# Kernel tuning notes

Measured on AMD Instinct MI355X. Metric: run time of the kernel, lower is better.

The kernel has to match this reference:

```python
import jax, jax.numpy as jnp
import numpy as np

D = 1024       # d_model
DR = 1024      # d_rec
FFN = 4096     # ffn_inner
K = 4          # conv_kernel
B, T = 2, 4096
CHUNK = 64
EPS = 1e-6


def setup_inputs() -> dict:
    key = jax.random.key(0)
    ks = jax.random.split(key, 8)
    s = lambda k, shape, scale: jax.random.normal(k, shape, jnp.float32) * scale
    db = np.zeros((DR,), np.float32)
    q = DR // 4
    db[:q] = -2.2
    db[q:3 * q] = 0.0
    db[3 * q:] = 4.6
    return {
        "x": s(ks[0], (B, T, D), 1.0),
        "pre_norm_w": jnp.ones((D,), jnp.float32),
        "conv_w": s(ks[1], (D, 1, K), 0.3),
        "conv_b": jnp.zeros((D,), jnp.float32),
        "w_a": s(ks[2], (DR, D), 0.02),
        "w_i": s(ks[3], (DR, D), 0.02),
        "w_v": s(ks[4], (DR, D), 0.02),
        "out_proj_w": s(ks[5], (D, DR), 0.02),
        "decay_bias": jnp.asarray(db),
        "ffn_norm_w": jnp.ones((D,), jnp.float32),
        "w_gate_up": s(ks[6], (2 * FFN, D), 0.02),
        "w_down": s(ks[7], (D, FFN), 0.02),
    }


def rmsnorm(x, w):
    return x * jax.lax.rsqrt(jnp.mean(x * x, axis=-1, keepdims=True) + EPS) * w


def lin(x, w):  # nn.Linear weight layout (out, in)
    return jnp.einsum('btd,od->bto', x, w)


def causal_conv(h, w, b):
    # depthwise causal conv: h (B,T,D), w (D,1,K)
    hc = jnp.transpose(h, (0, 2, 1))  # (B,D,T)
    out = jax.lax.conv_general_dilated(
        hc, w, window_strides=(1,), padding=[(K - 1, 0)],
        dimension_numbers=('NCH', 'OIH', 'NCH'), feature_group_count=D)
    return jnp.transpose(out, (0, 2, 1)) + b


def chunked_scan(a, v):
    b, s, d = a.shape
    pad = (-s) % CHUNK
    af = jnp.pad(a, ((0, 0), (0, pad), (0, 0)), constant_values=1.0)
    vf = jnp.pad(v, ((0, 0), (0, pad), (0, 0)))
    n = (s + pad) // CHUNK
    dc = af.reshape(b, n, CHUNK, d)
    vc = vf.reshape(b, n, CHUNK, d)
    cum_decay = jnp.exp(jnp.cumsum(jnp.log(jnp.clip(dc, 1e-10)), axis=2))
    intra = cum_decay * jnp.cumsum(vc / jnp.clip(cum_decay, 1e-10), axis=2)

    def step(state, xs):
        cd, it = xs  # (B,CHUNK,d) each
        cs = it + cd * state[:, None, :]
        return cs[:, -1], cs

    _, states = jax.lax.scan(
        step, jnp.zeros((b, d), jnp.float32),
        (jnp.transpose(cum_decay, (1, 0, 2, 3)), jnp.transpose(intra, (1, 0, 2, 3))))
    return jnp.transpose(states, (1, 0, 2, 3)).reshape(b, n * CHUNK, d)[:, :s]


def reference(x, pre_norm_w, conv_w, conv_b, w_a, w_i, w_v, out_proj_w,
              decay_bias, ffn_norm_w, w_gate_up, w_down):
    h = rmsnorm(x, pre_norm_w)
    h = causal_conv(h, conv_w, conv_b)
    a = jax.nn.sigmoid(lin(h, w_a) + decay_bias)
    i_gate = jax.nn.sigmoid(lin(h, w_i))
    v = lin(h, w_v)
    input_signal = jnp.sqrt(jnp.clip(1.0 - a * a, 1e-8)) * (i_gate * v)
    rec_out = chunked_scan(a, input_signal).astype(x.dtype)
    x = x + lin(rec_out, out_proj_w)
    hn = rmsnorm(x, ffn_norm_w)
    gu = lin(hn, w_gate_up)
    gate, up = gu[..., :FFN], gu[..., FFN:]
    x = x + lin(jax.nn.silu(gate) * up, w_down)
    return x
```

## Files before the change

### kernel.cpp

```cpp
#include <hip/hip_runtime.h>

typedef __bf16 bf16_t;
typedef bf16_t bf16x4 __attribute__((ext_vector_type(4)));
typedef bf16_t bf16x8 __attribute__((ext_vector_type(8)));
typedef float f32x4 __attribute__((ext_vector_type(4)));

#define DD 1024
#define TT 4096

__device__ __forceinline__ void gload16(const void* g, void* l) {
    __builtin_amdgcn_global_load_lds(
        (const __attribute__((address_space(1))) void*)g,
        (__attribute__((address_space(3))) void*)l, 16, 0, 0);
}

__global__ __launch_bounds__(256) void cvt3_k(const float* __restrict__ s0,
                                              const float* __restrict__ s1,
                                              const float* __restrict__ s2,
                                              bf16_t* __restrict__ d0,
                                              bf16_t* __restrict__ d1,
                                              bf16_t* __restrict__ d2) {
    const int i = (blockIdx.x * 256 + threadIdx.x) * 4;
    const float* s; bf16_t* d; int off;
    if (i < 1048576)            { s = s0; d = d0; off = i; }
    else if (i < 2097152)       { s = s1; d = d1; off = i - 1048576; }
    else                        { s = s2; d = d2; off = i - 2097152; }
    const float4 v = *(const float4*)(s + off);
    bf16x4 o;
    o[0] = (bf16_t)v.x; o[1] = (bf16_t)v.y; o[2] = (bf16_t)v.z; o[3] = (bf16_t)v.w;
    *(bf16x4*)(d + off) = o;
}

__global__ __launch_bounds__(256) void cvt_ilv2_k(const float* __restrict__ wi,
                                                  const float* __restrict__ wv,
                                                  bf16_t* __restrict__ wivb,
                                                  const float* __restrict__ wgu,
                                                  bf16_t* __restrict__ wgub) {
    const int i = (blockIdx.x * 256 + threadIdx.x) * 4;
    const float* src; bf16_t* dst; int idx;
    if (i < 2097152) {
        idx = i;
        const int rp = idx >> 10, k = idx & 1023, c = rp >> 1;
        src = ((rp & 1) ? wv : wi) + (long)c * 1024 + k;
        dst = wivb + idx;
    } else {
        idx = i - 2097152;
        const int rp = idx >> 10, k = idx & 1023, c = rp >> 1;
        src = ((rp & 1) ? (wgu + 4194304) : wgu) + (long)c * 1024 + k;
        dst = wgub + idx;
    }
    const float4 v = *(const float4*)src;
    bf16x4 o;
    o[0] = (bf16_t)v.x; o[1] = (bf16_t)v.y; o[2] = (bf16_t)v.z; o[3] = (bf16_t)v.w;
    *(bf16x4*)dst = o;
}

__global__ __launch_bounds__(256) void rmsnorm_k(const float* __restrict__ x,
                                                 const float* __restrict__ w,
                                                 bf16_t* __restrict__ ob) {
    const long row = blockIdx.x;
    const float* xr = x + row * DD;
    const int t4 = threadIdx.x * 4;
    float4 v = *(const float4*)(xr + t4);
    float s = v.x*v.x + v.y*v.y + v.z*v.z + v.w*v.w;
    #pragma unroll
    for (int off = 1; off < 64; off <<= 1) s += __shfl_xor(s, off);
    __shared__ float red[4];
    if ((threadIdx.x & 63) == 0) red[threadIdx.x >> 6] = s;
    __syncthreads();
    float tot = red[0] + red[1] + red[2] + red[3];
    float sc = rsqrtf(tot * (1.0f / DD) + 1e-6f);
    float4 wv = *(const float4*)(w + t4);
    bf16x4 o;
    o[0] = (bf16_t)(v.x*sc*wv.x); o[1] = (bf16_t)(v.y*sc*wv.y);
    o[2] = (bf16_t)(v.z*sc*wv.z); o[3] = (bf16_t)(v.w*sc*wv.w);
    *(bf16x4*)(ob + row * DD + t4) = o;
}

__global__ __launch_bounds__(256) void conv_k(const bf16_t* __restrict__ h,
                                              const float* __restrict__ cw,
                                              const float* __restrict__ cb,
                                              bf16_t* __restrict__ hc) {
    const long idx = (long)blockIdx.x * 256 + threadIdx.x;
    const int d = (int)(idx & (DD - 1));
    const long bt = idx >> 10;
    const int t = (int)(bt & (TT - 1));
    const float w0 = cw[d*4+0], w1 = cw[d*4+1], w2 = cw[d*4+2], w3 = cw[d*4+3];
    const bf16_t* hp = h + bt * DD + d;
    float acc = cb[d] + (float)hp[0] * w3;
    if (t >= 1) acc += (float)hp[-DD]     * w2;
    if (t >= 2) acc += (float)hp[-2*DD]   * w1;
    if (t >= 3) acc += (float)hp[-3*DD]   * w0;
    hc[idx] = (bf16_t)acc;
}

__global__ __launch_bounds__(256) void scan1_k(const bf16_t* __restrict__ ap,
                                               const bf16_t* __restrict__ sp,
                                               float* __restrict__ cd63,
                                               float* __restrict__ i63) {
    const int d = blockIdx.x * 256 + threadIdx.x;
    const int c = blockIdx.y;
    const int b = blockIdx.z;
    const long rowbase = (long)b * TT + (long)c * 64;
    float cd = 1.0f, rs = 0.0f;
    for (int t = 0; t < 64; t++) {
        const long off = (rowbase + t) * DD + d;
        const float a = (float)ap[off];
        const float s = (float)sp[off];
        const float sig = __builtin_amdgcn_sqrtf(fmaxf(1.0f - a * a, 1e-8f)) * s;
        cd *= fmaxf(a, 1e-10f);
        rs = fmaf(sig, __builtin_amdgcn_rcpf(fmaxf(cd, 1e-10f)), rs);
    }
    const long o = ((long)b * 64 + c) * DD + d;
    cd63[o] = cd;
    i63[o]  = cd * rs;
}

__global__ __launch_bounds__(256) void scan2_k(const float* __restrict__ cd63,
                                               const float* __restrict__ i63,
                                               float* __restrict__ carry_in) {
    const int g = blockIdx.x * 256 + threadIdx.x;
    const int b = g >> 10, d = g & (DD - 1);
    float st = 0.0f;
    for (int c = 0; c < 64; c++) {
        const long o = ((long)b * 64 + c) * DD + d;
        carry_in[o] = st;
        st = i63[o] + cd63[o] * st;
    }
}

__global__ __launch_bounds__(256) void scan3_k(const bf16_t* __restrict__ ap,
                                               const bf16_t* __restrict__ sp,
                                               const float* __restrict__ carry_in,
                                               bf16_t* __restrict__ rec) {
    const int d = blockIdx.x * 256 + threadIdx.x;
    const int c = blockIdx.y;
    const int b = blockIdx.z;
    const long rowbase = (long)b * TT + (long)c * 64;
    const float carry = carry_in[((long)b * 64 + c) * DD + d];
    float cd = 1.0f, rs = 0.0f;
    for (int t = 0; t < 64; t++) {
        const long off = (rowbase + t) * DD + d;
        const float a = (float)ap[off];
        const float s = (float)sp[off];
        const float sig = __builtin_amdgcn_sqrtf(fmaxf(1.0f - a * a, 1e-8f)) * s;
        cd *= fmaxf(a, 1e-10f);
        rs = fmaf(sig, __builtin_amdgcn_rcpf(fmaxf(cd, 1e-10f)), rs);
        rec[off] = (bf16_t)(cd * (rs + carry));
    }
}

enum { EPI_SIGB = 0, EPI_ADDRES = 1, EPI_IV = 2, EPI_GU = 3 };

template<int EPI, int NREP>
__global__ __launch_bounds__(512, 2) void gemm2p_k(const bf16_t* __restrict__ Ag,
                                                   const bf16_t* __restrict__ Bg,
                                                   int M, int N, int K,
                                                   float* outF, bf16_t* outB,
                                                   const float* aux, int ldc) {
    constexpr int BN  = NREP * 64;
    constexpr int ASZ = 16384;
    constexpr int BSZ = BN * 64;
    constexpr int BUF = ASZ + BSZ;
    extern __shared__ bf16_t smem[];
    const int tid = threadIdx.x;
    const int l = tid & 63;
    const int w = tid >> 6;
    const int wm = w >> 2, wn = w & 3;

    const int gx = gridDim.x;
    const int gy = gridDim.y;
    const int lin = blockIdx.y * gx + blockIdx.x;
    long row0, col0;
    if ((gy & 7) == 0) {
        const int rpc = gy >> 3;
        const int q = lin >> 3;
        row0 = (long)((lin & 7) * rpc + q % rpc) * 256;
        col0 = (long)(q / rpc) * (long)BN;
    } else {
        row0 = (long)blockIdx.y * 256;
        col0 = (long)blockIdx.x * BN;
    }

    const int srow = l >> 3;
    const int scol = ((l & 7) ^ srow) * 8;
    const long aBase = row0 + srow;
    const long bBase = col0 + srow;
    const int R0a = w * 32;
    const int R0b = w * (BN / 8);

    const int NT = K >> 6;
    f32x4 acc[8][NREP] = {};

    const int lq2 = (l >> 4) * 16;
    const int rA = wm * 128 + (l & 15);
    const int rB = wn * (NREP * 16) + (l & 15);
    const int eA0 = rA * 64 + ((lq2 ^ ((rA & 7) << 4)) >> 1);
    const int eB0 = ASZ + rB * 64 + ((lq2 ^ ((rB & 7) << 4)) >> 1);

    #define STAGE_A(tt, off)                                                          \
        { const long kgk = (long)(tt) * 64 + scol;                                    \
          _Pragma("unroll")                                                           \
          for (int i = 0; i < 4; i++)                                                 \
              gload16(Ag + (aBase + R0a + i * 8) * (long)K + kgk,                     \
                      &smem[(off) + (R0a + i * 8) * 64]); }
    #define STAGE_B(tt, off)                                                          \
        { const long kgk = (long)(tt) * 64 + scol;                                    \
          _Pragma("unroll")                                                           \
          for (int i = 0; i < NREP; i++)                                              \
              gload16(Bg + (bBase + R0b + i * 8) * (long)K + kgk,                     \
                      &smem[(off) + ASZ + (R0b + i * 8) * 64]); }

    STAGE_A(0, 0); STAGE_B(0, 0);
    STAGE_A(1, BUF); STAGE_B(1, BUF);
    if constexpr (NREP == 4) { asm volatile("s_waitcnt vmcnt(8)" ::: "memory"); }
    else                     { asm volatile("s_waitcnt vmcnt(6)" ::: "memory"); }
    asm volatile("s_barrier" ::: "memory");

    bf16x8 pA[2][4], pB[2][NREP];
    #pragma unroll
    for (int kk = 0; kk < 2; kk++) {
        const int xo = kk * 32;
        #pragma unroll
        for (int n = 0; n < NREP; n++)
            pB[kk][n] = *(const bf16x8*)&smem[(eB0 ^ xo) + n * 1024];
        #pragma unroll
        for (int m = 0; m < 4; m++)
            pA[kk][m] = *(const bf16x8*)&smem[(eA0 ^ xo) + m * 1024];
    }

    for (int t = 0; t < NT; t++) {
        const int co = (t & 1) ? BUF : 0;
        const int oo = BUF - co;
        bf16x8 a1[2][4];

        __builtin_amdgcn_s_setprio(1);
        #pragma unroll
        for (int kk = 0; kk < 2; kk++)
            #pragma unroll
            for (int m = 0; m < 4; m++)
                #pragma unroll
                for (int n = 0; n < NREP; n++)
                    acc[m][n] = __builtin_amdgcn_mfma_f32_16x16x32_bf16(pA[kk][m], pB[kk][n], acc[m][n], 0, 0, 0);
        __builtin_amdgcn_s_setprio(0);
        #pragma unroll
        for (int kk = 0; kk < 2; kk++) {
            const int xo = kk * 32;
            #pragma unroll
            for (int m = 0; m < 4; m++)
                a1[kk][m] = *(const bf16x8*)&smem[co + (eA0 ^ xo) + 4096 + m * 1024];
        }
        asm volatile("s_barrier" ::: "memory");

        if (t + 2 < NT) { STAGE_A(t + 2, co); STAGE_B(t + 2, co); }
        __builtin_amdgcn_s_setprio(1);
        #pragma unroll
        for (int kk = 0; kk < 2; kk++)
            #pragma unroll
            for (int m = 0; m < 4; m++)
                #pragma unroll
                for (int n = 0; n < NREP; n++)
                    acc[m + 4][n] = __builtin_amdgcn_mfma_f32_16x16x32_bf16(a1[kk][m], pB[kk][n], acc[m + 4][n], 0, 0, 0);
        __builtin_amdgcn_s_setprio(0);
        if (t + 2 < NT) {
            if constexpr (NREP == 4) { asm volatile("s_waitcnt vmcnt(8)" ::: "memory"); }
            else                     { asm volatile("s_waitcnt vmcnt(6)" ::: "memory"); }
        } else if (t + 1 < NT) {
            asm volatile("s_waitcnt vmcnt(0)" ::: "memory");
        }
        asm volatile("s_barrier" ::: "memory");
        if (t + 1 < NT) {
            #pragma unroll
            for (int kk = 0; kk < 2; kk++) {
                const int xo = kk * 32;
                #pragma unroll
                for (int n = 0; n < NREP; n++)
                    pB[kk][n] = *(const bf16x8*)&smem[oo + (eB0 ^ xo) + n * 1024];
                #pragma unroll
                for (int m = 0; m < 4; m++)
                    pA[kk][m] = *(const bf16x8*)&smem[oo + (eA0 ^ xo) + m * 1024];
            }
        }
    }
    #undef STAGE_A
    #undef STAGE_B

    #pragma unroll
    for (int m = 0; m < 8; m++) {
        const long r0 = row0 + wm * 128 + m * 16 + (l >> 4) * 4;
        #pragma unroll
        for (int n = 0; n < NREP; n++) {
            const long cc = col0 + wn * (NREP * 16) + n * 16 + (l & 15);
            f32x4 v = acc[m][n];
            #pragma unroll
            for (int j = 0; j < 4; j++) {
                const long r = r0 + j;
                const float xv = v[j];
                if (EPI == EPI_SIGB) {
                    outB[r * ldc + cc] = (bf16_t)(1.0f / (1.0f + __expf(-(xv + aux[cc]))));
                } else if (EPI == EPI_ADDRES) {
                    outF[r * ldc + cc] = xv + aux[r * ldc + cc];
                } else if (EPI == EPI_IV) {
                    const float px = __shfl_xor(xv, 1);
                    if ((l & 1) == 0)
                        outB[r * ldc + (cc >> 1)] = (bf16_t)(px / (1.0f + __expf(-xv)));
                } else {
                    const float px = __shfl_xor(xv, 1);
                    if ((l & 1) == 0)
                        outB[r * ldc + (cc >> 1)] = (bf16_t)(xv / (1.0f + __expf(-xv)) * px);
                }
            }
        }
    }
}

extern "C" void kernel_launch(void* const* d_in, const int* in_sizes, int n_in,
                              void* d_out, int out_size, void* d_ws, size_t ws_size,
                              hipStream_t stream) {
    const float* x   = (const float*)d_in[0];
    const float* pnw = (const float*)d_in[1];
    const float* cw  = (const float*)d_in[2];
    const float* cb  = (const float*)d_in[3];
    const float* wa  = (const float*)d_in[4];
    const float* wi  = (const float*)d_in[5];
    const float* wv  = (const float*)d_in[6];
    const float* wop = (const float*)d_in[7];
    const float* db  = (const float*)d_in[8];
    const float* fnw = (const float*)d_in[9];
    const float* wgu = (const float*)d_in[10];
    const float* wdn = (const float*)d_in[11];
    float* out = (float*)d_out;

    char* ws = (char*)d_ws;
    bf16_t* wab   = (bf16_t*)(ws + 0);
    bf16_t* wivb  = (bf16_t*)(ws + 2097152);
    bf16_t* wopb  = (bf16_t*)(ws + 6291456);
    bf16_t* wgub  = (bf16_t*)(ws + 8388608);
    bf16_t* wdnb  = (bf16_t*)(ws + 25165824);
    bf16_t* hb    = (bf16_t*)(ws + 33554432);
    bf16_t* hn    = hb;
    bf16_t* hc    = (bf16_t*)(ws + 50331648);
    bf16_t* rec   = hc;
    bf16_t* a_b   = (bf16_t*)(ws + 67108864);
    bf16_t* s_b   = (bf16_t*)(ws + 100663296);
    bf16_t* act   = (bf16_t*)(ws + 67108864);
    float*  cd63  = (float*)(ws + 134217728);
    float*  i63   = (float*)(ws + 134742016);
    float*  carry = (float*)(ws + 135266304);

    const int LDS4 = 131072;
    const int LDS2 = 98304;
    hipFuncSetAttribute((const void*)gemm2p_k<EPI_SIGB, 2>,   hipFuncAttributeMaxDynamicSharedMemorySize, LDS2);
    hipFuncSetAttribute((const void*)gemm2p_k<EPI_IV, 4>,     hipFuncAttributeMaxDynamicSharedMemorySize, LDS4);
    hipFuncSetAttribute((const void*)gemm2p_k<EPI_ADDRES, 2>, hipFuncAttributeMaxDynamicSharedMemorySize, LDS2);
    hipFuncSetAttribute((const void*)gemm2p_k<EPI_GU, 4>,     hipFuncAttributeMaxDynamicSharedMemorySize, LDS4);

    cvt3_k    <<<6144, 256, 0, stream>>>(wa, wop, wdn, wab, wopb, wdnb);
    cvt_ilv2_k<<<10240, 256, 0, stream>>>(wi, wv, wivb, wgu, wgub);

    rmsnorm_k<<<8192, 256, 0, stream>>>(x, pnw, hb);
    conv_k<<<32768, 256, 0, stream>>>(hb, cw, cb, hc);

    gemm2p_k<EPI_SIGB, 2><<<dim3(8, 32), 512, LDS2, stream>>>(hc, wab,  8192, 1024, 1024,
                                                              nullptr, a_b, db, 1024);
    gemm2p_k<EPI_IV, 4>  <<<dim3(8, 32), 512, LDS4, stream>>>(hc, wivb, 8192, 2048, 1024,
                                                              nullptr, s_b, nullptr, 1024);
    scan1_k<<<dim3(4, 64, 2), 256, 0, stream>>>(a_b, s_b, cd63, i63);
    scan2_k<<<8, 256, 0, stream>>>(cd63, i63, carry);
    scan3_k<<<dim3(4, 64, 2), 256, 0, stream>>>(a_b, s_b, carry, rec);

    gemm2p_k<EPI_ADDRES, 2><<<dim3(8, 32), 512, LDS2, stream>>>(rec, wopb, 8192, 1024, 1024,
                                                                out, nullptr, x, 1024);
    rmsnorm_k<<<8192, 256, 0, stream>>>(out, fnw, hn);
    gemm2p_k<EPI_GU, 4><<<dim3(32, 32), 512, LDS4, stream>>>(hn, wgub, 8192, 8192, 1024,
                                                             nullptr, act, nullptr, 4096);
    gemm2p_k<EPI_ADDRES, 2><<<dim3(8, 32), 512, LDS2, stream>>>(act, wdnb, 8192, 1024, 4096,
                                                                out, nullptr, out, 1024);
}
```

Baseline: 436.8 us.

## Add 128x128-tile GEMM kernel for N=1024 projections to raise CU occupancy

Adds a new 256-thread GEMM kernel with 128x128 tiles, 64 KB LDS and two blocks per CU. It stages A and B separately with double buffering and uses an XCD-aware tile swizzle. The three GEMMs with N=1024 (decay gate, out-projection, down-projection) move to it, launching 512 blocks instead of 256. This is meant to fix poor CU fill from too few large tiles on 256 CUs, at the cost of less data reuse per tile and more total memory traffic.

```diff
diff --git a/kernel.cpp b/kernel.cpp
--- a/kernel.cpp
+++ b/kernel.cpp
@@ -314,6 +314,139 @@
     }
 }
 
+template<int EPI>
+__global__ __launch_bounds__(256, 2) void gemm2b_k(const bf16_t* __restrict__ Ag,
+                                                   const bf16_t* __restrict__ Bg,
+                                                   int M, int N, int K,
+                                                   float* outF, bf16_t* outB,
+                                                   const float* aux, int ldc) {
+    constexpr int ASZ = 8192;
+    constexpr int BUF = 16384;
+    extern __shared__ bf16_t smem[];
+    const int tid = threadIdx.x;
+    const int l = tid & 63;
+    const int w = tid >> 6;
+    const int wm = w >> 1, wn = w & 1;
+
+    const int gx = gridDim.x;
+    const int gy = gridDim.y;
+    const int lin = blockIdx.y * gx + blockIdx.x;
+    long row0, col0;
+    if ((gy & 7) == 0) {
+        const int rpc = gy >> 3;
+        const int q = lin >> 3;
+        row0 = (long)((lin & 7) * rpc + q % rpc) * 128;
+        col0 = (long)(q / rpc) * 128;
+    } else {
+        row0 = (long)blockIdx.y * 128;
+        col0 = (long)blockIdx.x * 128;
+    }
+
+    const int srow = l >> 3;
+    const int scol = ((l & 7) ^ srow) * 8;
+    const long aBase = row0 + srow;
+    const long bBase = col0 + srow;
+    const int R0 = w * 32;
+
+    const int NT = K >> 6;
+    f32x4 acc[4][4] = {};
+
+    const int lq2 = (l >> 4) * 16;
+    const int rA = wm * 64 + (l & 15);
+    const int rB = wn * 64 + (l & 15);
+    const int eA0 = rA * 64 + ((lq2 ^ ((rA & 7) << 4)) >> 1);
+    const int eB0 = ASZ + rB * 64 + ((lq2 ^ ((rB & 7) << 4)) >> 1);
+
+    #define ST_A(tt, off, i)                                                        \
+        gload16(Ag + (aBase + R0 + (i) * 8) * (long)K + (long)(tt) * 64 + scol,     \
+                &smem[(off) + (R0 + (i) * 8) * 64])
+    #define ST_B(tt, off, i)                                                        \
+        gload16(Bg + (bBase + R0 + (i) * 8) * (long)K + (long)(tt) * 64 + scol,     \
+                &smem[(off) + ASZ + (R0 + (i) * 8) * 64])
+    #define BAR asm volatile("s_barrier" ::: "memory")
+
+    #pragma unroll
+    for (int i = 0; i < 4; i++) ST_B(0, 0, i);
+    #pragma unroll
+    for (int i = 0; i < 4; i++) ST_A(0, 0, i);
+    #pragma unroll
+    for (int i = 0; i < 4; i++) ST_B(1, BUF, i);
+    asm volatile("s_waitcnt vmcnt(4)" ::: "memory");
+    BAR;
+
+    for (int t = 0; t < NT; t++) {
+        const int cur = (t & 1) * BUF;
+        const int oth = BUF - cur;
+        bf16x8 bk[4], af[4];
+
+        #pragma unroll
+        for (int n = 0; n < 4; n++)
+            bk[n] = *(const bf16x8*)&smem[cur + eB0 + n * 1024];
+        #pragma unroll
+        for (int m = 0; m < 4; m++)
+            af[m] = *(const bf16x8*)&smem[cur + eA0 + m * 1024];
+        if (t + 1 < NT) {
+            #pragma unroll
+            for (int i = 0; i < 4; i++) ST_A(t + 1, oth, i);
+        }
+        BAR;
+        __builtin_amdgcn_s_setprio(1);
+        #pragma unroll
+        for (int m = 0; m < 4; m++)
+            #pragma unroll
+            for (int n = 0; n < 4; n++)
+                acc[m][n] = __builtin_amdgcn_mfma_f32_16x16x32_bf16(af[m], bk[n], acc[m][n], 0, 0, 0);
+        __builtin_amdgcn_s_setprio(0);
+        BAR;
+
+        #pragma unroll
+        for (int n = 0; n < 4; n++)
+            bk[n] = *(const bf16x8*)&smem[cur + (eB0 ^ 32) + n * 1024];
+        #pragma unroll
+        for (int m = 0; m < 4; m++)
+            af[m] = *(const bf16x8*)&smem[cur + (eA0 ^ 32) + m * 1024];
+        BAR;
+        __builtin_amdgcn_s_setprio(1);
+        #pragma unroll
+        for (int m = 0; m < 4; m++)
+            #pragma unroll
+            for (int n = 0; n < 4; n++)
+                acc[m][n] = __builtin_amdgcn_mfma_f32_16x16x32_bf16(af[m], bk[n], acc[m][n], 0, 0, 0);
+        __builtin_amdgcn_s_setprio(0);
+        if (t + 2 < NT) {
+            #pragma unroll
+            for (int i = 0; i < 4; i++) ST_B(t + 2, cur, i);
+            asm volatile("s_waitcnt vmcnt(4)" ::: "memory");
+        } else {
+            asm volatile("s_waitcnt vmcnt(0)" ::: "memory");
+        }
+        BAR;
+    }
+    #undef ST_A
+    #undef ST_B
+    #undef BAR
+
+    #pragma unroll
+    for (int m = 0; m < 4; m++) {
+        const long r0 = row0 + wm * 64 + m * 16 + (l >> 4) * 4;
+        #pragma unroll
+        for (int n = 0; n < 4; n++) {
+            const long cc = col0 + wn * 64 + n * 16 + (l & 15);
+            f32x4 v = acc[m][n];
+            #pragma unroll
+            for (int j = 0; j < 4; j++) {
+                const long r = r0 + j;
+                const float xv = v[j];
+                if (EPI == EPI_SIGB) {
+                    outB[r * ldc + cc] = (bf16_t)(1.0f / (1.0f + __expf(-(xv + aux[cc]))));
+                } else {
+                    outF[r * ldc + cc] = xv + aux[r * ldc + cc];
+                }
+            }
+        }
+    }
+}
+
 extern "C" void kernel_launch(void* const* d_in, const int* in_sizes, int n_in,
                               void* d_out, int out_size, void* d_ws, size_t ws_size,
                               hipStream_t stream) {
@@ -349,11 +482,11 @@
     float*  carry = (float*)(ws + 135266304);
 
     const int LDS4 = 131072;
-    const int LDS2 = 98304;
-    hipFuncSetAttribute((const void*)gemm2p_k<EPI_SIGB, 2>,   hipFuncAttributeMaxDynamicSharedMemorySize, LDS2);
-    hipFuncSetAttribute((const void*)gemm2p_k<EPI_IV, 4>,     hipFuncAttributeMaxDynamicSharedMemorySize, LDS4);
-    hipFuncSetAttribute((const void*)gemm2p_k<EPI_ADDRES, 2>, hipFuncAttributeMaxDynamicSharedMemorySize, LDS2);
-    hipFuncSetAttribute((const void*)gemm2p_k<EPI_GU, 4>,     hipFuncAttributeMaxDynamicSharedMemorySize, LDS4);
+    const int LDSB = 65536;
+    hipFuncSetAttribute((const void*)gemm2p_k<EPI_IV, 4>,   hipFuncAttributeMaxDynamicSharedMemorySize, LDS4);
+    hipFuncSetAttribute((const void*)gemm2p_k<EPI_GU, 4>,   hipFuncAttributeMaxDynamicSharedMemorySize, LDS4);
+    hipFuncSetAttribute((const void*)gemm2b_k<EPI_SIGB>,    hipFuncAttributeMaxDynamicSharedMemorySize, LDSB);
+    hipFuncSetAttribute((const void*)gemm2b_k<EPI_ADDRES>,  hipFuncAttributeMaxDynamicSharedMemorySize, LDSB);
 
     cvt3_k    <<<6144, 256, 0, stream>>>(wa, wop, wdn, wab, wopb, wdnb);
     cvt_ilv2_k<<<10240, 256, 0, stream>>>(wi, wv, wivb, wgu, wgub);
@@ -361,19 +494,19 @@
     rmsnorm_k<<<8192, 256, 0, stream>>>(x, pnw, hb);
     conv_k<<<32768, 256, 0, stream>>>(hb, cw, cb, hc);
 
-    gemm2p_k<EPI_SIGB, 2><<<dim3(8, 32), 512, LDS2, stream>>>(hc, wab,  8192, 1024, 1024,
-                                                              nullptr, a_b, db, 1024);
-    gemm2p_k<EPI_IV, 4>  <<<dim3(8, 32), 512, LDS4, stream>>>(hc, wivb, 8192, 2048, 1024,
-                                                              nullptr, s_b, nullptr, 1024);
+    gemm2b_k<EPI_SIGB><<<dim3(8, 64), 256, LDSB, stream>>>(hc, wab, 8192, 1024, 1024,
+                                                           nullptr, a_b, db, 1024);
+    gemm2p_k<EPI_IV, 4><<<dim3(8, 32), 512, LDS4, stream>>>(hc, wivb, 8192, 2048, 1024,
+                                                            nullptr, s_b, nullptr, 1024);
     scan1_k<<<dim3(4, 64, 2), 256, 0, stream>>>(a_b, s_b, cd63, i63);
     scan2_k<<<8, 256, 0, stream>>>(cd63, i63, carry);
     scan3_k<<<dim3(4, 64, 2), 256, 0, stream>>>(a_b, s_b, carry, rec);
 
-    gemm2p_k<EPI_ADDRES, 2><<<dim3(8, 32), 512, LDS2, stream>>>(rec, wopb, 8192, 1024, 1024,
-                                                                out, nullptr, x, 1024);
+    gemm2b_k<EPI_ADDRES><<<dim3(8, 64), 256, LDSB, stream>>>(rec, wopb, 8192, 1024, 1024,
+                                                             out, nullptr, x, 1024);
     rmsnorm_k<<<8192, 256, 0, stream>>>(out, fnw, hn);
     gemm2p_k<EPI_GU, 4><<<dim3(32, 32), 512, LDS4, stream>>>(hn, wgub, 8192, 8192, 1024,
                                                              nullptr, act, nullptr, 4096);
-    gemm2p_k<EPI_ADDRES, 2><<<dim3(8, 32), 512, LDS2, stream>>>(act, wdnb, 8192, 1024, 4096,
-                                                                out, nullptr, out, 1024);
-}
+    gemm2b_k<EPI_ADDRES><<<dim3(8, 64), 256, LDSB, stream>>>(act, wdnb, 8192, 1024, 4096,
+                                                             out, nullptr, out, 1024);
+}
```

After: 441.6 us. No clear change (+1.1%).
